# Performance work log

Hardware: AMD Instinct MI355X
Metric: run time of the kernel (lower is better)

## Reference

```python
import jax, jax.numpy as jnp
import numpy as np

B, INPUT, MEM, CELL, HEADS, K = 32, 512, 32768, 64, 1, 16
VIS = K + 1  # visible_size = sparse_reads + 1


def setup_inputs() -> dict:
    key = jax.random.key(0)
    ks = jax.random.split(key, 8)
    n = lambda k, s: jax.random.normal(k, s, jnp.float32)
    scale = 0.05  # small init so tanh/sigmoid stay in useful range
    return {
        "xi": n(ks[0], (B, INPUT)),
        "memory": n(ks[1], (B, MEM, CELL)),
        "least_used_mem": jax.random.randint(ks[2], (B, 1), 0, MEM),
        "W_rq": n(ks[3], (HEADS * CELL, INPUT)) * scale,
        "b_rq": jnp.zeros((HEADS * CELL,), jnp.float32),
        "W_wv": n(ks[4], (CELL, INPUT)) * scale,
        "b_wv": jnp.zeros((CELL,), jnp.float32),
        "W_ig": n(ks[5], (VIS, INPUT)) * scale,
        "b_ig": jnp.zeros((VIS,), jnp.float32),
        "W_wg": n(ks[6], (1, INPUT)) * scale,
        "b_wg": jnp.zeros((1,), jnp.float32),
    }


def reference(xi, memory, least_used_mem, W_rq, b_rq, W_wv, b_wv, W_ig, b_ig, W_wg, b_wg):
    b = xi.shape[0]
    # interface transforms (independent_linears=True path)
    read_query = jnp.tanh(xi @ W_rq.T + b_rq).reshape(b, HEADS, CELL)
    write_vector = jnp.tanh(xi @ W_wv.T + b_wv).reshape(b, 1, CELL)
    interpolation_gate = jax.nn.sigmoid(xi @ W_ig.T + b_ig)          # [b, VIS]
    write_gate = jax.nn.sigmoid(xi @ W_wg.T + b_wg)                  # [b, 1]

    # kNN search over memory (torch.topk fallback path of read_from_sparse_memory)
    sims = jnp.einsum("bhc,bmc->bhm", read_query, memory)            # [b, H, MEM]
    _, idx = jax.lax.top_k(sims, K)                                  # [b, H, K]
    read_positions = jnp.concatenate([idx.reshape(b, -1), least_used_mem], axis=1)  # [b, VIS]

    # gather visible memory cells
    visible_memory = jnp.take_along_axis(memory, read_positions[:, :, None], axis=1)  # [b, VIS, CELL]

    # attention over visible cells
    rw = jax.nn.softmax(jnp.einsum("bhc,bvc->bhv", read_query, visible_memory), axis=2)  # [b, H, VIS]
    read_vectors = jnp.einsum("bhv,bvc->bhc", rw, visible_memory)    # [b, H, CELL]
    rw_flat = rw.sum(axis=1)                                         # [b, VIS]

    # scatter read weights into full memory-sized vector (torch scatter_ = set)
    read_weights = jnp.zeros((b, MEM), xi.dtype).at[
        jnp.arange(b)[:, None], read_positions
    ].set(rw_flat)                                                   # [b, MEM]

    return read_vectors, read_weights, visible_memory, write_vector, interpolation_gate, write_gate
```

## Files before the change

kernel.cpp:

```cpp
#include <hip/hip_runtime.h>
#include <cstdint>
#include <cstddef>
#include <cfloat>
#include <cmath>

#define NB    32
#define NIN   512
#define NMEM  32768
#define NCELL 64
#define NVIS  17
#define NK    16
#define NBLK  32
#define RPB   (NMEM / NBLK)

#define OFF_RV  0
#define OFF_RW  2048
#define OFF_VIS 1050624
#define OFF_WV  1085440
#define OFF_IG  1087488
#define OFF_WG  1088032

#define SCR_RQ  0
#define SCR_CV  64
#define SCR_CI  576

__global__ __launch_bounds__(256) void kA(
    const float* __restrict__ xi,
    const float* __restrict__ Wrq, const float* __restrict__ brq,
    const float* __restrict__ Wwv, const float* __restrict__ bwv,
    const float* __restrict__ Wig, const float* __restrict__ big,
    const float* __restrict__ Wwg, const float* __restrict__ bwg,
    float* __restrict__ out)
{
    int b = blockIdx.x;
    int tid = threadIdx.x;
    float* rq_scr = out + OFF_RW + (size_t)b * NMEM + SCR_RQ;
    __shared__ float sxi[NIN];
    for (int i = tid; i < NIN; i += 256)
        sxi[i] = xi[(size_t)b * NIN + i];
    __syncthreads();
    int g = tid >> 3, sub = tid & 7;
    for (int it = 0; it < 5; ++it) {
        int row = it * 32 + g;
        if (row < 146) {
            const float* W; float bias; int kind, r;
            if (row < 64)       { r = row;       W = Wrq + (size_t)r * NIN; bias = brq[r]; kind = 0; }
            else if (row < 128) { r = row - 64;  W = Wwv + (size_t)r * NIN; bias = bwv[r]; kind = 1; }
            else if (row < 145) { r = row - 128; W = Wig + (size_t)r * NIN; bias = big[r]; kind = 2; }
            else                { r = 0;         W = Wwg;                   bias = bwg[0]; kind = 3; }
            float acc = 0.f;
            const float* wp = W   + sub * 64;
            const float* xp = sxi + sub * 64;
            for (int j = 0; j < 64; ++j)
                acc = fmaf(wp[j], xp[j], acc);
            acc += __shfl_xor(acc, 1);
            acc += __shfl_xor(acc, 2);
            acc += __shfl_xor(acc, 4);
            if (sub == 0) {
                float x = acc + bias;
                if (kind == 0)      rq_scr[r] = tanhf(x);
                else if (kind == 1) out[OFF_WV + b * NCELL + r] = tanhf(x);
                else if (kind == 2) out[OFF_IG + b * NVIS + r]  = 1.f / (1.f + expf(-x));
                else                out[OFF_WG + b]             = 1.f / (1.f + expf(-x));
            }
        }
    }
}

__global__ __launch_bounds__(256) void kB(
    const float* __restrict__ mem, float* __restrict__ out)
{
    int b   = blockIdx.y;
    int blk = blockIdx.x;
    int tid = threadIdx.x;
    int w = tid >> 6, lane = tid & 63;
    int sub = lane & 7;
    float* rwrow = out + OFF_RW + (size_t)b * NMEM;
    __shared__ float ssim[4][256];
    __shared__ float wcv[64];
    __shared__ int   wci[64];

    float rqv[8];
    for (int e = 0; e < 8; ++e) rqv[e] = rwrow[SCR_RQ + sub * 8 + e];

    const float* mb = mem + (size_t)b * NMEM * NCELL + (size_t)(blk * RPB + w * 256) * NCELL;

    for (int it = 0; it < 32; ++it) {
        int lr = it * 8 + (lane >> 3);
        const float* rp = mb + (size_t)lr * NCELL + sub * 8;
        float4 a = *(const float4*)rp;
        float4 d = *(const float4*)(rp + 4);
        float acc = 0.f;
        acc = fmaf(a.x, rqv[0], acc); acc = fmaf(a.y, rqv[1], acc);
        acc = fmaf(a.z, rqv[2], acc); acc = fmaf(a.w, rqv[3], acc);
        acc = fmaf(d.x, rqv[4], acc); acc = fmaf(d.y, rqv[5], acc);
        acc = fmaf(d.z, rqv[6], acc); acc = fmaf(d.w, rqv[7], acc);
        acc += __shfl_xor(acc, 1);
        acc += __shfl_xor(acc, 2);
        acc += __shfl_xor(acc, 4);
        if (sub == 0) ssim[w][lr] = acc;
    }
    __syncthreads();

    int gbase = blk * RPB + w * 256;
    float v[4]; int gi[4];
    for (int j = 0; j < 4; ++j) {
        v[j]  = ssim[w][lane * 4 + j];
        gi[j] = gbase + lane * 4 + j;
    }
    for (int r = 0; r < NK; ++r) {
        float bv = v[0]; int bi = gi[0];
        for (int j = 1; j < 4; ++j)
            if (v[j] > bv || (v[j] == bv && gi[j] < bi)) { bv = v[j]; bi = gi[j]; }
        for (int off = 32; off >= 1; off >>= 1) {
            float ov = __shfl_xor(bv, off); int oi = __shfl_xor(bi, off);
            if (ov > bv || (ov == bv && oi < bi)) { bv = ov; bi = oi; }
        }
        for (int j = 0; j < 4; ++j)
            if (gi[j] == bi) { v[j] = -FLT_MAX; gi[j] = 0x7fffffff; }
        if (lane == 0) { wcv[w * 16 + r] = bv; wci[w * 16 + r] = bi; }
    }
    __syncthreads();

    if (w == 0) {
        float mv2 = wcv[lane]; int mi2 = wci[lane];
        float* ovp = rwrow + SCR_CV + blk * NK;
        int*   oip = (int*)(rwrow + SCR_CI) + blk * NK;
        for (int r = 0; r < NK; ++r) {
            float bv = mv2; int bi = mi2;
            for (int off = 32; off >= 1; off >>= 1) {
                float ov = __shfl_xor(bv, off); int oi = __shfl_xor(bi, off);
                if (ov > bv || (ov == bv && oi < bi)) { bv = ov; bi = oi; }
            }
            if (mi2 == bi) { mv2 = -FLT_MAX; mi2 = 0x7fffffff; }
            if (lane == 0) { ovp[r] = bv; oip[r] = bi; }
        }
    }
}

__global__ __launch_bounds__(256) void kC(
    const float* __restrict__ mem, const int* __restrict__ lum,
    float* __restrict__ out)
{
    int b = blockIdx.x;
    int tid = threadIdx.x;
    int w = tid >> 6, lane = tid & 63;
    float* rwrow = out + OFF_RW + (size_t)b * NMEM;
    __shared__ float lv[NBLK * NK];
    __shared__ int   li[NBLK * NK];
    __shared__ int   pos_s[NVIS];
    __shared__ float sc_s[NVIS];
    __shared__ float rw_s[NVIS];
    __shared__ float pacc[4][NCELL];

    for (int j = 0; j < 2; ++j) {
        int e = tid * 2 + j;
        lv[e] = rwrow[SCR_CV + e];
        li[e] = ((const int*)(rwrow + SCR_CI))[e];
    }
    __syncthreads();

    if (w == 0) {
        float v[8]; int gi[8];
        for (int j = 0; j < 8; ++j) { v[j] = lv[lane * 8 + j]; gi[j] = li[lane * 8 + j]; }
        for (int r = 0; r < NK; ++r) {
            float bv = v[0]; int bi = gi[0];
            for (int j = 1; j < 8; ++j)
                if (v[j] > bv || (v[j] == bv && gi[j] < bi)) { bv = v[j]; bi = gi[j]; }
            for (int off = 32; off >= 1; off >>= 1) {
                float ov = __shfl_xor(bv, off); int oi = __shfl_xor(bi, off);
                if (ov > bv || (ov == bv && oi < bi)) { bv = ov; bi = oi; }
            }
            for (int j = 0; j < 8; ++j)
                if (gi[j] == bi) { v[j] = -FLT_MAX; gi[j] = 0x7fffffff; }
            if (lane == 0) { pos_s[r] = bi & (NMEM - 1); sc_s[r] = bv; }
        }
        int p16 = lum[b] & (NMEM - 1);
        float x = mem[((size_t)b * NMEM + p16) * NCELL + lane] * rwrow[SCR_RQ + lane];
        for (int off = 32; off >= 1; off >>= 1) x += __shfl_xor(x, off);
        if (lane == 0) { pos_s[NK] = p16; sc_s[NK] = x; }
    }
    __syncthreads();

    if (w == 0) {
        float sc = (lane < NVIS) ? sc_s[lane] : -FLT_MAX;
        float mx = sc;
        for (int off = 32; off >= 1; off >>= 1) mx = fmaxf(mx, __shfl_xor(mx, off));
        float e = (lane < NVIS) ? expf(sc - mx) : 0.f;
        float sum = e;
        for (int off = 32; off >= 1; off >>= 1) sum += __shfl_xor(sum, off);
        if (lane < NVIS) rw_s[lane] = e / sum;
    }
    __syncthreads();

    for (int it = 0; it < 128; ++it)
        rwrow[it * 256 + tid] = 0.f;

    float acc = 0.f;
    for (int vv = w; vv < NVIS; vv += 4) {
        int p = pos_s[vv] & (NMEM - 1);
        float hv = mem[((size_t)b * NMEM + p) * NCELL + lane];
        out[OFF_VIS + ((size_t)b * NVIS + vv) * NCELL + lane] = hv;
        acc = fmaf(rw_s[vv], hv, acc);
    }
    pacc[w][lane] = acc;
    __syncthreads();

    if (tid < NCELL) {
        float s = pacc[0][tid] + pacc[1][tid] + pacc[2][tid] + pacc[3][tid];
        out[OFF_RV + b * NCELL + tid] = s;
    }
    if (tid < NVIS) {
        int p = pos_s[tid] & (NMEM - 1);
        bool dup = (tid < NK) && (p == pos_s[NK]);
        if (!dup) rwrow[p] = rw_s[tid];
    }
}

extern "C" void kernel_launch(void* const* d_in, const int* in_sizes, int n_in,
                              void* d_out, int out_size, void* d_ws, size_t ws_size,
                              hipStream_t stream)
{
    const float* xi  = (const float*)d_in[0];
    const float* mem = (const float*)d_in[1];
    const int*   lum = (const int*)d_in[2];
    const float* Wrq = (const float*)d_in[3];
    const float* brq = (const float*)d_in[4];
    const float* Wwv = (const float*)d_in[5];
    const float* bwv = (const float*)d_in[6];
    const float* Wig = (const float*)d_in[7];
    const float* big = (const float*)d_in[8];
    const float* Wwg = (const float*)d_in[9];
    const float* bwg = (const float*)d_in[10];
    float* out = (float*)d_out;

    kA<<<dim3(NB), dim3(256), 0, stream>>>(xi, Wrq, brq, Wwv, bwv, Wig, big, Wwg, bwg, out);
    kB<<<dim3(NBLK, NB), dim3(256), 0, stream>>>(mem, out);
    kC<<<dim3(NB), dim3(256), 0, stream>>>(mem, lum, out);
}
```

Measured before the change: 102.3 us.

## Move scratch to workspace, zero read weights in kB, parallelize kA rows

Scratch data (read query and per-block top-k candidates) moves from the read_weights output region into the workspace buffer when one is available. Zeroing the 32768-wide read_weights rows then happens spread across kB's 1024 blocks instead of serially in kC's 32 blocks. kA now launches a 2D grid so the 146 linear rows are split across 5x more blocks. If the workspace is missing or too small, the code falls back to the old in-output scratch layout.

```diff
diff --git a/kernel.cpp b/kernel.cpp
--- a/kernel.cpp
+++ b/kernel.cpp
@@ -23,6 +23,7 @@
 #define SCR_RQ  0
 #define SCR_CV  64
 #define SCR_CI  576
+#define SCR_STRIDE_WS 1088
 
 __global__ __launch_bounds__(256) void kA(
     const float* __restrict__ xi,
@@ -30,58 +31,64 @@
     const float* __restrict__ Wwv, const float* __restrict__ bwv,
     const float* __restrict__ Wig, const float* __restrict__ big,
     const float* __restrict__ Wwg, const float* __restrict__ bwg,
+    float* __restrict__ scr_base, int scr_stride,
     float* __restrict__ out)
 {
     int b = blockIdx.x;
     int tid = threadIdx.x;
-    float* rq_scr = out + OFF_RW + (size_t)b * NMEM + SCR_RQ;
+    float* rq_scr = scr_base + (size_t)b * scr_stride + SCR_RQ;
     __shared__ float sxi[NIN];
     for (int i = tid; i < NIN; i += 256)
         sxi[i] = xi[(size_t)b * NIN + i];
     __syncthreads();
     int g = tid >> 3, sub = tid & 7;
-    for (int it = 0; it < 5; ++it) {
-        int row = it * 32 + g;
-        if (row < 146) {
-            const float* W; float bias; int kind, r;
-            if (row < 64)       { r = row;       W = Wrq + (size_t)r * NIN; bias = brq[r]; kind = 0; }
-            else if (row < 128) { r = row - 64;  W = Wwv + (size_t)r * NIN; bias = bwv[r]; kind = 1; }
-            else if (row < 145) { r = row - 128; W = Wig + (size_t)r * NIN; bias = big[r]; kind = 2; }
-            else                { r = 0;         W = Wwg;                   bias = bwg[0]; kind = 3; }
-            float acc = 0.f;
-            const float* wp = W   + sub * 64;
-            const float* xp = sxi + sub * 64;
-            for (int j = 0; j < 64; ++j)
-                acc = fmaf(wp[j], xp[j], acc);
-            acc += __shfl_xor(acc, 1);
-            acc += __shfl_xor(acc, 2);
-            acc += __shfl_xor(acc, 4);
-            if (sub == 0) {
-                float x = acc + bias;
-                if (kind == 0)      rq_scr[r] = tanhf(x);
-                else if (kind == 1) out[OFF_WV + b * NCELL + r] = tanhf(x);
-                else if (kind == 2) out[OFF_IG + b * NVIS + r]  = 1.f / (1.f + expf(-x));
-                else                out[OFF_WG + b]             = 1.f / (1.f + expf(-x));
-            }
+    int row = blockIdx.y * 32 + g;
+    if (row < 146) {
+        const float* W; float bias; int kind, r;
+        if (row < 64)       { r = row;       W = Wrq + (size_t)r * NIN; bias = brq[r]; kind = 0; }
+        else if (row < 128) { r = row - 64;  W = Wwv + (size_t)r * NIN; bias = bwv[r]; kind = 1; }
+        else if (row < 145) { r = row - 128; W = Wig + (size_t)r * NIN; bias = big[r]; kind = 2; }
+        else                { r = 0;         W = Wwg;                   bias = bwg[0]; kind = 3; }
+        float acc = 0.f;
+        const float* wp = W   + sub * 64;
+        const float* xp = sxi + sub * 64;
+        for (int j = 0; j < 64; ++j)
+            acc = fmaf(wp[j], xp[j], acc);
+        acc += __shfl_xor(acc, 1);
+        acc += __shfl_xor(acc, 2);
+        acc += __shfl_xor(acc, 4);
+        if (sub == 0) {
+            float x = acc + bias;
+            if (kind == 0)      rq_scr[r] = tanhf(x);
+            else if (kind == 1) out[OFF_WV + b * NCELL + r] = tanhf(x);
+            else if (kind == 2) out[OFF_IG + b * NVIS + r]  = 1.f / (1.f + expf(-x));
+            else                out[OFF_WG + b]             = 1.f / (1.f + expf(-x));
         }
     }
 }
 
 __global__ __launch_bounds__(256) void kB(
-    const float* __restrict__ mem, float* __restrict__ out)
+    const float* __restrict__ mem,
+    float* __restrict__ scr_base, int scr_stride, int kb_zero,
+    float* __restrict__ out)
 {
     int b   = blockIdx.y;
     int blk = blockIdx.x;
     int tid = threadIdx.x;
     int w = tid >> 6, lane = tid & 63;
     int sub = lane & 7;
-    float* rwrow = out + OFF_RW + (size_t)b * NMEM;
+    float* scr = scr_base + (size_t)b * scr_stride;
     __shared__ float ssim[4][256];
     __shared__ float wcv[64];
     __shared__ int   wci[64];
 
+    if (kb_zero) {
+        float4 z; z.x = z.y = z.z = z.w = 0.f;
+        ((float4*)(out + OFF_RW + (size_t)b * NMEM + blk * RPB))[tid] = z;
+    }
+
     float rqv[8];
-    for (int e = 0; e < 8; ++e) rqv[e] = rwrow[SCR_RQ + sub * 8 + e];
+    for (int e = 0; e < 8; ++e) rqv[e] = scr[SCR_RQ + sub * 8 + e];
 
     const float* mb = mem + (size_t)b * NMEM * NCELL + (size_t)(blk * RPB + w * 256) * NCELL;
 
@@ -124,8 +131,8 @@
 
     if (w == 0) {
         float mv2 = wcv[lane]; int mi2 = wci[lane];
-        float* ovp = rwrow + SCR_CV + blk * NK;
-        int*   oip = (int*)(rwrow + SCR_CI) + blk * NK;
+        float* ovp = scr + SCR_CV + blk * NK;
+        int*   oip = (int*)(scr + SCR_CI) + blk * NK;
         for (int r = 0; r < NK; ++r) {
             float bv = mv2; int bi = mi2;
             for (int off = 32; off >= 1; off >>= 1) {
@@ -140,12 +147,14 @@
 
 __global__ __launch_bounds__(256) void kC(
     const float* __restrict__ mem, const int* __restrict__ lum,
+    const float* __restrict__ scr_base, int scr_stride, int kc_zero,
     float* __restrict__ out)
 {
     int b = blockIdx.x;
     int tid = threadIdx.x;
     int w = tid >> 6, lane = tid & 63;
     float* rwrow = out + OFF_RW + (size_t)b * NMEM;
+    const float* scr = scr_base + (size_t)b * scr_stride;
     __shared__ float lv[NBLK * NK];
     __shared__ int   li[NBLK * NK];
     __shared__ int   pos_s[NVIS];
@@ -155,8 +164,8 @@
 
     for (int j = 0; j < 2; ++j) {
         int e = tid * 2 + j;
-        lv[e] = rwrow[SCR_CV + e];
-        li[e] = ((const int*)(rwrow + SCR_CI))[e];
+        lv[e] = scr[SCR_CV + e];
+        li[e] = ((const int*)(scr + SCR_CI))[e];
     }
     __syncthreads();
 
@@ -176,7 +185,7 @@
             if (lane == 0) { pos_s[r] = bi & (NMEM - 1); sc_s[r] = bv; }
         }
         int p16 = lum[b] & (NMEM - 1);
-        float x = mem[((size_t)b * NMEM + p16) * NCELL + lane] * rwrow[SCR_RQ + lane];
+        float x = mem[((size_t)b * NMEM + p16) * NCELL + lane] * scr[SCR_RQ + lane];
         for (int off = 32; off >= 1; off >>= 1) x += __shfl_xor(x, off);
         if (lane == 0) { pos_s[NK] = p16; sc_s[NK] = x; }
     }
@@ -193,8 +202,10 @@
     }
     __syncthreads();
 
-    for (int it = 0; it < 128; ++it)
-        rwrow[it * 256 + tid] = 0.f;
+    if (kc_zero) {
+        for (int it = 0; it < 128; ++it)
+            rwrow[it * 256 + tid] = 0.f;
+    }
 
     float acc = 0.f;
     for (int vv = w; vv < NVIS; vv += 4) {
@@ -234,7 +245,14 @@
     const float* bwg = (const float*)d_in[10];
     float* out = (float*)d_out;
 
-    kA<<<dim3(NB), dim3(256), 0, stream>>>(xi, Wrq, brq, Wwv, bwv, Wig, big, Wwg, bwg, out);
-    kB<<<dim3(NBLK, NB), dim3(256), 0, stream>>>(mem, out);
-    kC<<<dim3(NB), dim3(256), 0, stream>>>(mem, lum, out);
-}
+    bool use_ws = (d_ws != nullptr) && (ws_size >= (size_t)NB * SCR_STRIDE_WS * 4);
+    float* scrb = use_ws ? (float*)d_ws : out + OFF_RW;
+    int    scrs = use_ws ? SCR_STRIDE_WS : NMEM;
+    int    kb_zero = use_ws ? 1 : 0;
+    int    kc_zero = use_ws ? 0 : 1;
+
+    kA<<<dim3(NB, 5), dim3(256), 0, stream>>>(xi, Wrq, brq, Wwv, bwv, Wig, big,
+                                              Wwg, bwg, scrb, scrs, out);
+    kB<<<dim3(NBLK, NB), dim3(256), 0, stream>>>(mem, scrb, scrs, kb_zero, out);
+    kC<<<dim3(NB), dim3(256), 0, stream>>>(mem, lum, scrb, scrs, kc_zero, out);
+}
```

Result: faster. 91.10 us (-10.9%).
